# Performance work log

Hardware: AMD Instinct MI355X
Metric: run time of the kernel (lower is better)

## Reference

```python
import jax, jax.numpy as jnp
import numpy as np

B, L, D = 16, 4096, 256
DEP = 50


def setup_inputs() -> dict:
    key = jax.random.key(0)
    ks = jax.random.split(key, 20)
    s = 1.0 / np.sqrt(D)
    inp = {
        "inputs": jax.random.normal(ks[0], (B, L, D), jnp.float32),
        "parent_positions": jax.random.randint(ks[1], (B, L), 0, L, jnp.int32),
        "sentence_deps": jax.random.randint(ks[2], (B, L), 0, DEP, jnp.int32),
        "attention_mask": jax.random.randint(ks[3], (B, L), 0, 2, jnp.int32),
        # linear weights stored [in, out]
        "W_loop": jax.random.uniform(ks[4], (D, D), jnp.float32, -s, s),
        "b_loop": jnp.zeros((D,), jnp.float32),
        "W_child": jax.random.uniform(ks[5], (D, D), jnp.float32, -s, s),
        "b_child": jnp.zeros((D,), jnp.float32),
        "W_parent": jax.random.uniform(ks[6], (D, D), jnp.float32, -s, s),
        "b_parent": jnp.zeros((D,), jnp.float32),
        "w_loop_g": jax.random.uniform(ks[7], (D, 1), jnp.float32, -s, s),
        "b_loop_g": jnp.zeros((1,), jnp.float32),
        "w_child_g": jax.random.uniform(ks[8], (D, 1), jnp.float32, -s, s),
        "b_child_g": jnp.zeros((1,), jnp.float32),
        "w_parent_g": jax.random.uniform(ks[9], (D, 1), jnp.float32, -s, s),
        "b_parent_g": jnp.zeros((1,), jnp.float32),
        "E_pw": jax.random.normal(ks[10], (DEP, D), jnp.float32),
        "E_cw": jax.random.normal(ks[11], (DEP, D), jnp.float32),
        "E_pg": jax.random.normal(ks[12], (DEP, 1), jnp.float32),
        "E_cg": jax.random.normal(ks[13], (DEP, 1), jnp.float32),
    }
    return inp


def _scatter_add_children(idx, vals):
    # idx: [L] parent index per child; vals: [L, D]
    # out[p] = sum_{i: idx[i]==p} vals[i]  (== one_hot(idx).T @ vals)
    return jnp.zeros((L, vals.shape[-1]), vals.dtype).at[idx].add(vals)


def reference(inputs, parent_positions, sentence_deps, attention_mask,
              W_loop, b_loop, W_child, b_child, W_parent, b_parent,
              w_loop_g, b_loop_g, w_child_g, b_child_g, w_parent_g, b_parent_g,
              E_pw, E_cw, E_pg, E_cg):
    x = inputs
    n_iterator = 1
    for _ in range(n_iterator):
        # gather parent node states: [B, L, D]
        par = jnp.take_along_axis(x, parent_positions[:, :, None].astype(jnp.int32), axis=1)
        deps = sentence_deps
        loop_gate = jax.nn.sigmoid(x @ w_loop_g + b_loop_g)                       # [B,L,1]
        par_gate = jax.nn.sigmoid(x @ w_parent_g + b_parent_g + E_pg[deps])       # [B,L,1]
        child_gate = jax.nn.sigmoid(x @ w_child_g + b_child_g + E_cg[deps])       # [B,L,1]
        loop_conv = loop_gate * (x @ W_loop + b_loop)
        parent_conv = par_gate * (par @ W_parent + b_parent + E_pw[deps])
        child_mat = child_gate * (x @ W_child + b_child + E_cw[deps])
        # masked parents (pad positions point to 0), then scatter-add children
        mpp = jnp.where(attention_mask != 0, parent_positions, 0)
        child_conv = jax.vmap(_scatter_add_children)(mpp, child_mat)
        x = loop_conv + parent_conv + child_conv
    return x * attention_mask[:, :, None].astype(x.dtype)
```

## Files before the change

kernel.cpp:

```cpp
#include <hip/hip_runtime.h>
#include <hip/hip_bf16.h>
#include <stdint.h>

#define B_ 16
#define L_ 4096
#define D_ 256
#define M_ (B_*L_)
#define N_ 768

typedef __attribute__((ext_vector_type(8))) short bf16x8;
typedef __attribute__((ext_vector_type(4))) float f32x4;
typedef __attribute__((ext_vector_type(4))) int i32x4;

__device__ __forceinline__ float bf2f(unsigned short u) {
  union { unsigned int i; float f; } v; v.i = ((unsigned int)u) << 16; return v.f;
}
__device__ __forceinline__ unsigned short f2bf(float f) {
  __hip_bfloat16 h = __float2bfloat16(f);
  return *reinterpret_cast<unsigned short*>(&h);
}
__device__ __forceinline__ void async16(const void* g, void* l) {
  __builtin_amdgcn_global_load_lds((const __attribute__((address_space(1))) void*)g,
                                   (__attribute__((address_space(3))) void*)l, 16, 0, 0);
}
__device__ __forceinline__ float sigmoidf_(float z) {
  return 1.f / (1.f + __expf(-z));
}

__global__ __launch_bounds__(256) void k_gates(
    const float* __restrict__ x, const int* __restrict__ deps,
    const int* __restrict__ parent, const int* __restrict__ mask,
    const float* __restrict__ wlg, const float* __restrict__ blg,
    const float* __restrict__ wcg, const float* __restrict__ bcg,
    const float* __restrict__ wpg, const float* __restrict__ bpg,
    const float* __restrict__ Epg, const float* __restrict__ Ecg,
    unsigned short* __restrict__ xb, float4* __restrict__ gates,
    int* __restrict__ cnt)
{
  const int lane = threadIdx.x & 63;
  const int gw = (blockIdx.x * 256 + threadIdx.x) >> 6;
  const float4 wl4 = ((const float4*)wlg)[lane];
  const float4 wc4 = ((const float4*)wcg)[lane];
  const float4 wp4 = ((const float4*)wpg)[lane];
  const float bl0 = blg[0], bc0 = bcg[0], bp0 = bpg[0];
  for (int t = 0; t < 8; ++t) {
    const int i = gw * 8 + t;
    const int b = i >> 12;
    float4 xv = ((const float4*)x)[(size_t)i * 64 + lane];
    float sl = xv.x * wl4.x + xv.y * wl4.y + xv.z * wl4.z + xv.w * wl4.w;
    float sc = xv.x * wc4.x + xv.y * wc4.y + xv.z * wc4.z + xv.w * wc4.w;
    float sp = xv.x * wp4.x + xv.y * wp4.y + xv.z * wp4.z + xv.w * wp4.w;
    #pragma unroll
    for (int o = 32; o; o >>= 1) {
      sl += __shfl_xor(sl, o);
      sc += __shfl_xor(sc, o);
      sp += __shfl_xor(sp, o);
    }
    ushort4 u;
    u.x = f2bf(xv.x); u.y = f2bf(xv.y); u.z = f2bf(xv.z); u.w = f2bf(xv.w);
    ((ushort4*)xb)[(size_t)i * 64 + lane] = u;
    if (lane == 0) {
      int d = deps[i];
      float gl = sigmoidf_(sl + bl0);
      float gp = sigmoidf_(sp + bp0 + Epg[d]);
      float gc = sigmoidf_(sc + bc0 + Ecg[d]);
      gates[i] = make_float4(gl, gp, gc, 0.f);
      int mi = mask[i];
      if (mi) {
        int p = parent[i];
        if (p > 0 && mask[(b << 12) + p]) atomicAdd(&cnt[(b << 12) + p], 1);
      }
    }
  }
}

__global__ __launch_bounds__(256) void k_weights(
    const float* __restrict__ Wl, const float* __restrict__ Wp,
    const float* __restrict__ Wc, unsigned short* __restrict__ WbT)
{
  const int n = blockIdx.x;
  const int k = threadIdx.x;
  const float* W = (n < 256) ? Wl : ((n < 512) ? Wp : Wc);
  const int nn = n & 255;
  WbT[(size_t)n * 256 + k] = f2bf(W[(size_t)k * 256 + nn]);
}

__global__ __launch_bounds__(256) void k_scan(
    const int* __restrict__ cnt, int* __restrict__ off, int* __restrict__ cur)
{
  const int b = blockIdx.x, t = threadIdx.x;
  const int base = (b << 12) + t * 16;
  int v, pre[16], s = 0;
  #pragma unroll
  for (int j = 0; j < 16; ++j) { v = cnt[base + j]; pre[j] = s; s += v; }
  __shared__ int tot[256];
  tot[t] = s;
  __syncthreads();
  for (int o = 1; o < 256; o <<= 1) {
    int x = (t >= o) ? tot[t - o] : 0;
    __syncthreads();
    tot[t] += x;
    __syncthreads();
  }
  const int bexc = tot[t] - s;
  #pragma unroll
  for (int j = 0; j < 16; ++j) {
    off[base + j] = bexc + pre[j];
    cur[base + j] = bexc + pre[j];
  }
}

__global__ __launch_bounds__(256) void k_fill(
    const int* __restrict__ parent, const int* __restrict__ mask,
    int* __restrict__ cur, int* __restrict__ lists)
{
  const int i = blockIdx.x * 256 + threadIdx.x;
  const int b = i >> 12;
  if (!mask[i]) return;
  const int p = parent[i];
  if (p == 0) return;
  if (!mask[(b << 12) + p]) return;
  const int pos = atomicAdd(&cur[(b << 12) + p], 1);
  lists[(b << 12) + pos] = i;
}

__global__ __launch_bounds__(256) void k_gemm(
    const unsigned short* __restrict__ A,
    const unsigned short* __restrict__ Bt,
    unsigned short* __restrict__ Y)
{
  __shared__ unsigned short sh[2 * 128 * 64];
  unsigned short* lA = sh;
  unsigned short* lB = sh + 128 * 64;
  const int tid = threadIdx.x;
  const int wid = tid >> 6, lane = tid & 63;
  const int wm = wid >> 1, wn = wid & 1;
  const int mb = blockIdx.x, nb = blockIdx.y;

  f32x4 acc[4][4] = {};
  const unsigned short* Ag = A + (size_t)mb * 128 * 256;
  const unsigned short* Bg = Bt + (size_t)nb * 128 * 256;
  const int srow = wid * 8 + (lane >> 3);
  const int scol = (lane & 7) * 8;

  for (int kb = 0; kb < 256; kb += 64) {
    #pragma unroll
    for (int s = 0; s < 4; ++s) {
      char* dA = (char*)lA + s * 4096 + wid * 1024 + lane * 16;
      char* dB = (char*)lB + s * 4096 + wid * 1024 + lane * 16;
      async16(Ag + (size_t)(s * 32 + srow) * 256 + kb + scol, dA);
      async16(Bg + (size_t)(s * 32 + srow) * 256 + kb + scol, dB);
    }
    __syncthreads();
    #pragma unroll
    for (int kk = 0; kk < 64; kk += 32) {
      const int ko = kk + (lane >> 4) * 8;
      bf16x8 af[4], bv[4];
      #pragma unroll
      for (int m = 0; m < 4; ++m)
        af[m] = *(const bf16x8*)&lA[(wm * 64 + m * 16 + (lane & 15)) * 64 + ko];
      #pragma unroll
      for (int n = 0; n < 4; ++n)
        bv[n] = *(const bf16x8*)&lB[(wn * 64 + n * 16 + (lane & 15)) * 64 + ko];
      #pragma unroll
      for (int m = 0; m < 4; ++m)
        #pragma unroll
        for (int n = 0; n < 4; ++n)
          acc[m][n] = __builtin_amdgcn_mfma_f32_16x16x32_bf16(af[m], bv[n], acc[m][n], 0, 0, 0);
    }
    __syncthreads();
  }

  #pragma unroll
  for (int m = 0; m < 4; ++m)
    #pragma unroll
    for (int n = 0; n < 4; ++n)
      #pragma unroll
      for (int r = 0; r < 4; ++r)
        sh[(wm * 64 + m * 16 + (lane >> 4) * 4 + r) * 128 + wn * 64 + n * 16 + (lane & 15)]
            = f2bf(acc[m][n][r]);
  __syncthreads();
  #pragma unroll
  for (int s = 0; s < 8; ++s) {
    const int o = s * 4096 + tid * 16;
    const int row = o >> 8;
    const int colu = (o & 255) >> 1;
    *(i32x4*)&Y[(size_t)(mb * 128 + row) * 768 + nb * 128 + colu] =
        *(const i32x4*)((const char*)sh + o);
  }
}

__global__ __launch_bounds__(256) void k_fused(
    const unsigned short* __restrict__ Y, const float4* __restrict__ gates,
    const int* __restrict__ parent, const int* __restrict__ deps,
    const int* __restrict__ mask, const int* __restrict__ cnt,
    const int* __restrict__ off, const int* __restrict__ lists,
    const float* __restrict__ b_loop, const float* __restrict__ b_parent,
    const float* __restrict__ b_child,
    const float* __restrict__ Epw, const float* __restrict__ Ecw,
    float* __restrict__ out)
{
  const int lane = threadIdx.x & 63;
  const int i = blockIdx.x * 4 + (threadIdx.x >> 6);
  const int b = i >> 12;
  float4* orow = (float4*)(out + (size_t)i * 256) + lane;
  if (!mask[i]) { *orow = make_float4(0.f, 0.f, 0.f, 0.f); return; }

  const float4 g = gates[i];
  const int p = parent[i], d = deps[i];
  const float4 bl = ((const float4*)b_loop)[lane];
  const float4 bp = ((const float4*)b_parent)[lane];
  const ushort4 yl = ((const ushort4*)(Y + (size_t)i * 768))[lane];
  const ushort4 z  = ((const ushort4*)(Y + (size_t)((b << 12) + p) * 768 + 256))[lane];
  const float4 e   = ((const float4*)Epw)[d * 64 + lane];
  float4 o;
  o.x = g.x * (bf2f(yl.x) + bl.x) + g.y * (bf2f(z.x) + bp.x + e.x);
  o.y = g.x * (bf2f(yl.y) + bl.y) + g.y * (bf2f(z.y) + bp.y + e.y);
  o.z = g.x * (bf2f(yl.z) + bl.z) + g.y * (bf2f(z.z) + bp.z + e.z);
  o.w = g.x * (bf2f(yl.w) + bl.w) + g.y * (bf2f(z.w) + bp.w + e.w);

  const int n = cnt[i];
  if (n) {
    const int o0 = off[i];
    const float4 bc = ((const float4*)b_child)[lane];
    for (int k = 0; k < n; ++k) {
      const int c = lists[(b << 12) + o0 + k];
      const float gc = ((const float*)gates)[c * 4 + 2];
      const int dc = deps[c];
      const ushort4 yc = ((const ushort4*)(Y + (size_t)c * 768 + 512))[lane];
      const float4 ec = ((const float4*)Ecw)[dc * 64 + lane];
      o.x += gc * (bf2f(yc.x) + bc.x + ec.x);
      o.y += gc * (bf2f(yc.y) + bc.y + ec.y);
      o.z += gc * (bf2f(yc.z) + bc.z + ec.z);
      o.w += gc * (bf2f(yc.w) + bc.w + ec.w);
    }
  }
  *orow = o;
}

__global__ __launch_bounds__(256) void k_row0a(
    const unsigned short* __restrict__ Y, const float4* __restrict__ gates,
    const int* __restrict__ parent, const int* __restrict__ deps,
    const int* __restrict__ mask, const float* __restrict__ b_child,
    const float* __restrict__ Ecw, float4* __restrict__ partial)
{
  const int blk = blockIdx.x;
  const int b = blk >> 6;
  const int lane = threadIdx.x & 63;
  const int wid = threadIdx.x >> 6;
  float4 acc = make_float4(0.f, 0.f, 0.f, 0.f);
  if (mask[b << 12]) {
    const float4 bc = ((const float4*)b_child)[lane];
    const int tbase = (b << 12) + (blk & 63) * 64 + wid * 16;
    for (int t = 0; t < 16; ++t) {
      const int i = tbase + t;
      const int mi = mask[i];
      const int p = parent[i];
      if (mi && p != 0) continue;
      const float gc = ((const float*)gates)[i * 4 + 2];
      const int d = deps[i];
      const ushort4 yc = ((const ushort4*)(Y + (size_t)i * 768 + 512))[lane];
      const float4 ec = ((const float4*)Ecw)[d * 64 + lane];
      acc.x += gc * (bf2f(yc.x) + bc.x + ec.x);
      acc.y += gc * (bf2f(yc.y) + bc.y + ec.y);
      acc.z += gc * (bf2f(yc.z) + bc.z + ec.z);
      acc.w += gc * (bf2f(yc.w) + bc.w + ec.w);
    }
  }
  __shared__ float4 red[4][64];
  red[wid][lane] = acc;
  __syncthreads();
  if (wid == 0) {
    float4 a0 = red[0][lane], a1 = red[1][lane], a2 = red[2][lane], a3 = red[3][lane];
    a0.x += a1.x + a2.x + a3.x;
    a0.y += a1.y + a2.y + a3.y;
    a0.z += a1.z + a2.z + a3.z;
    a0.w += a1.w + a2.w + a3.w;
    partial[blk * 64 + lane] = a0;
  }
}

__global__ __launch_bounds__(64) void k_row0b(
    const int* __restrict__ mask, const float4* __restrict__ partial,
    float* __restrict__ out)
{
  const int b = blockIdx.x;
  if (!mask[b << 12]) return;
  const int t = threadIdx.x;
  float4 acc = make_float4(0.f, 0.f, 0.f, 0.f);
  for (int k = 0; k < 64; ++k) {
    const float4 v = partial[(b * 64 + k) * 64 + t];
    acc.x += v.x; acc.y += v.y; acc.z += v.z; acc.w += v.w;
  }
  float4* orow = (float4*)(out + (size_t)(b << 12) * 256) + t;
  float4 o = *orow;
  o.x += acc.x; o.y += acc.y; o.z += acc.z; o.w += acc.w;
  *orow = o;
}

extern "C" void kernel_launch(void* const* d_in, const int* in_sizes, int n_in,
                              void* d_out, int out_size, void* d_ws, size_t ws_size,
                              hipStream_t stream) {
  const float* x        = (const float*)d_in[0];
  const int*   parent   = (const int*)d_in[1];
  const int*   deps     = (const int*)d_in[2];
  const int*   mask     = (const int*)d_in[3];
  const float* W_loop   = (const float*)d_in[4];
  const float* b_loop   = (const float*)d_in[5];
  const float* W_child  = (const float*)d_in[6];
  const float* b_child  = (const float*)d_in[7];
  const float* W_parent = (const float*)d_in[8];
  const float* b_parent = (const float*)d_in[9];
  const float* wlg      = (const float*)d_in[10];
  const float* blg      = (const float*)d_in[11];
  const float* wcg      = (const float*)d_in[12];
  const float* bcg      = (const float*)d_in[13];
  const float* wpg      = (const float*)d_in[14];
  const float* bpg      = (const float*)d_in[15];
  const float* Epw      = (const float*)d_in[16];
  const float* Ecw      = (const float*)d_in[17];
  const float* Epg      = (const float*)d_in[18];
  const float* Ecg      = (const float*)d_in[19];
  float* out = (float*)d_out;

  char* ws = (char*)d_ws;
  unsigned short* xb  = (unsigned short*)ws;
  float4* partial     = (float4*)ws;
  unsigned short* WbT = (unsigned short*)(ws + 33554432);
  float4* gates       = (float4*)(ws + 33947648);
  unsigned short* Yv  = (unsigned short*)(ws + 34996224);
  int* cnt            = (int*)(ws + 135659520);
  int* off            = (int*)(ws + 135921664);
  int* cur            = (int*)(ws + 136183808);
  int* lists          = (int*)(ws + 136445952);

  hipMemsetAsync(cnt, 0, 262144, stream);
  k_gates<<<2048, 256, 0, stream>>>(x, deps, parent, mask, wlg, blg, wcg, bcg,
                                    wpg, bpg, Epg, Ecg, xb, gates, cnt);
  k_weights<<<768, 256, 0, stream>>>(W_loop, W_parent, W_child, WbT);
  k_scan<<<16, 256, 0, stream>>>(cnt, off, cur);
  k_fill<<<256, 256, 0, stream>>>(parent, mask, cur, lists);
  dim3 gg(512, 6, 1);
  k_gemm<<<gg, 256, 0, stream>>>(xb, WbT, Yv);
  k_row0a<<<1024, 256, 0, stream>>>(Yv, gates, parent, deps, mask, b_child,
                                    Ecw, partial);
  k_fused<<<16384, 256, 0, stream>>>(Yv, gates, parent, deps, mask, cnt, off,
                                     lists, b_loop, b_parent, b_child,
                                     Epw, Ecw, out);
  k_row0b<<<16, 64, 0, stream>>>(mask, partial, out);
}
```

Baseline: 263.8 us.

## Merge preprocessing kernels, build child lists in LDS, reorder GEMM grid

Measured after the change: 343.4 us. +30.1%, slower.

```diff
diff --git a/kernel.cpp b/kernel.cpp
--- a/kernel.cpp
+++ b/kernel.cpp
@@ -27,25 +27,89 @@
   return 1.f / (1.f + __expf(-z));
 }
 
-__global__ __launch_bounds__(256) void k_gates(
+__global__ __launch_bounds__(256) void k_pre(
     const float* __restrict__ x, const int* __restrict__ deps,
     const int* __restrict__ parent, const int* __restrict__ mask,
     const float* __restrict__ wlg, const float* __restrict__ blg,
     const float* __restrict__ wcg, const float* __restrict__ bcg,
     const float* __restrict__ wpg, const float* __restrict__ bpg,
     const float* __restrict__ Epg, const float* __restrict__ Ecg,
+    const float* __restrict__ Wl, const float* __restrict__ Wp,
+    const float* __restrict__ Wc,
     unsigned short* __restrict__ xb, float4* __restrict__ gates,
-    int* __restrict__ cnt)
+    unsigned short* __restrict__ WbT,
+    int* __restrict__ cnt, int* __restrict__ off, int* __restrict__ lists,
+    int* __restrict__ counter)
 {
-  const int lane = threadIdx.x & 63;
-  const int gw = (blockIdx.x * 256 + threadIdx.x) >> 6;
+  __shared__ int hist[4096];
+  __shared__ int tot[256];
+  const int bx = blockIdx.x;
+  const int tid = threadIdx.x;
+
+  if (bx >= 2048) {
+    if (bx < 2816) {
+      const int n = bx - 2048;
+      const float* W = (n < 256) ? Wl : ((n < 512) ? Wp : Wc);
+      WbT[(size_t)n * 256 + tid] = f2bf(W[(size_t)tid * 256 + (n & 255)]);
+    } else if (bx < 2832) {
+      const int b = bx - 2816;
+      const int base = b << 12;
+      #pragma unroll
+      for (int j = 0; j < 16; ++j) hist[tid + j * 256] = 0;
+      __syncthreads();
+      for (int j = 0; j < 16; ++j) {
+        const int i = base + j * 256 + tid;
+        if (mask[i]) {
+          const int p = parent[i];
+          if (p > 0 && mask[base + p]) atomicAdd(&hist[p], 1);
+        }
+      }
+      __syncthreads();
+      int v[16], s = 0;
+      #pragma unroll
+      for (int j = 0; j < 16; ++j) { v[j] = hist[tid * 16 + j]; s += v[j]; }
+      tot[tid] = s;
+      __syncthreads();
+      for (int o = 1; o < 256; o <<= 1) {
+        int xx = (tid >= o) ? tot[tid - o] : 0;
+        __syncthreads();
+        tot[tid] += xx;
+        __syncthreads();
+      }
+      int run = tot[tid] - s;
+      #pragma unroll
+      for (int j = 0; j < 16; ++j) {
+        const int k = tid * 16 + j;
+        cnt[base + k] = v[j];
+        off[base + k] = run;
+        hist[k] = run;
+        run += v[j];
+      }
+      __syncthreads();
+      for (int j = 0; j < 16; ++j) {
+        const int i = base + j * 256 + tid;
+        if (mask[i]) {
+          const int p = parent[i];
+          if (p > 0 && mask[base + p]) {
+            const int pos = atomicAdd(&hist[p], 1);
+            lists[base + pos] = i;
+          }
+        }
+      }
+    } else {
+      if (tid == 0) *counter = 0;
+    }
+    return;
+  }
+
+  const int lane = tid & 63;
+  const int gw = (bx * 256 + tid) >> 6;
   const float4 wl4 = ((const float4*)wlg)[lane];
   const float4 wc4 = ((const float4*)wcg)[lane];
   const float4 wp4 = ((const float4*)wpg)[lane];
   const float bl0 = blg[0], bc0 = bcg[0], bp0 = bpg[0];
   for (int t = 0; t < 8; ++t) {
     const int i = gw * 8 + t;
-    const int b = i >> 12;
     float4 xv = ((const float4*)x)[(size_t)i * 64 + lane];
     float sl = xv.x * wl4.x + xv.y * wl4.y + xv.z * wl4.z + xv.w * wl4.w;
     float sc = xv.x * wc4.x + xv.y * wc4.y + xv.z * wc4.z + xv.w * wc4.w;
@@ -65,63 +129,8 @@
       float gp = sigmoidf_(sp + bp0 + Epg[d]);
       float gc = sigmoidf_(sc + bc0 + Ecg[d]);
       gates[i] = make_float4(gl, gp, gc, 0.f);
-      int mi = mask[i];
-      if (mi) {
-        int p = parent[i];
-        if (p > 0 && mask[(b << 12) + p]) atomicAdd(&cnt[(b << 12) + p], 1);
-      }
-    }
-  }
-}
-
-__global__ __launch_bounds__(256) void k_weights(
-    const float* __restrict__ Wl, const float* __restrict__ Wp,
-    const float* __restrict__ Wc, unsigned short* __restrict__ WbT)
-{
-  const int n = blockIdx.x;
-  const int k = threadIdx.x;
-  const float* W = (n < 256) ? Wl : ((n < 512) ? Wp : Wc);
-  const int nn = n & 255;
-  WbT[(size_t)n * 256 + k] = f2bf(W[(size_t)k * 256 + nn]);
-}
-
-__global__ __launch_bounds__(256) void k_scan(
-    const int* __restrict__ cnt, int* __restrict__ off, int* __restrict__ cur)
-{
-  const int b = blockIdx.x, t = threadIdx.x;
-  const int base = (b << 12) + t * 16;
-  int v, pre[16], s = 0;
-  #pragma unroll
-  for (int j = 0; j < 16; ++j) { v = cnt[base + j]; pre[j] = s; s += v; }
-  __shared__ int tot[256];
-  tot[t] = s;
-  __syncthreads();
-  for (int o = 1; o < 256; o <<= 1) {
-    int x = (t >= o) ? tot[t - o] : 0;
-    __syncthreads();
-    tot[t] += x;
-    __syncthreads();
-  }
-  const int bexc = tot[t] - s;
-  #pragma unroll
-  for (int j = 0; j < 16; ++j) {
-    off[base + j] = bexc + pre[j];
-    cur[base + j] = bexc + pre[j];
-  }
-}
-
-__global__ __launch_bounds__(256) void k_fill(
-    const int* __restrict__ parent, const int* __restrict__ mask,
-    int* __restrict__ cur, int* __restrict__ lists)
-{
-  const int i = blockIdx.x * 256 + threadIdx.x;
-  const int b = i >> 12;
-  if (!mask[i]) return;
-  const int p = parent[i];
-  if (p == 0) return;
-  if (!mask[(b << 12) + p]) return;
-  const int pos = atomicAdd(&cur[(b << 12) + p], 1);
-  lists[(b << 12) + pos] = i;
+    }
+  }
 }
 
 __global__ __launch_bounds__(256) void k_gemm(
@@ -135,7 +144,8 @@
   const int tid = threadIdx.x;
   const int wid = tid >> 6, lane = tid & 63;
   const int wm = wid >> 1, wn = wid & 1;
-  const int mb = blockIdx.x, nb = blockIdx.y;
+  const int bid = blockIdx.x;
+  const int mb = bid / 6, nb = bid % 6;
 
   f32x4 acc[4][4] = {};
   const unsigned short* Ag = A + (size_t)mb * 128 * 256;
@@ -238,11 +248,12 @@
   *orow = o;
 }
 
-__global__ __launch_bounds__(256) void k_row0a(
+__global__ __launch_bounds__(256) void k_row0(
     const unsigned short* __restrict__ Y, const float4* __restrict__ gates,
     const int* __restrict__ parent, const int* __restrict__ deps,
     const int* __restrict__ mask, const float* __restrict__ b_child,
-    const float* __restrict__ Ecw, float4* __restrict__ partial)
+    const float* __restrict__ Ecw, float4* __restrict__ partial,
+    int* __restrict__ counter, float* __restrict__ out)
 {
   const int blk = blockIdx.x;
   const int b = blk >> 6;
@@ -268,6 +279,7 @@
     }
   }
   __shared__ float4 red[4][64];
+  __shared__ int lastflag;
   red[wid][lane] = acc;
   __syncthreads();
   if (wid == 0) {
@@ -278,24 +290,26 @@
     a0.w += a1.w + a2.w + a3.w;
     partial[blk * 64 + lane] = a0;
   }
-}
-
-__global__ __launch_bounds__(64) void k_row0b(
-    const int* __restrict__ mask, const float4* __restrict__ partial,
-    float* __restrict__ out)
-{
-  const int b = blockIdx.x;
-  if (!mask[b << 12]) return;
-  const int t = threadIdx.x;
-  float4 acc = make_float4(0.f, 0.f, 0.f, 0.f);
-  for (int k = 0; k < 64; ++k) {
-    const float4 v = partial[(b * 64 + k) * 64 + t];
-    acc.x += v.x; acc.y += v.y; acc.z += v.z; acc.w += v.w;
-  }
-  float4* orow = (float4*)(out + (size_t)(b << 12) * 256) + t;
-  float4 o = *orow;
-  o.x += acc.x; o.y += acc.y; o.z += acc.z; o.w += acc.w;
-  *orow = o;
+  __threadfence();
+  __syncthreads();
+  if (threadIdx.x == 0)
+    lastflag = (atomicAdd(counter, 1) == 1023);
+  __syncthreads();
+  if (!lastflag) return;
+  __threadfence();
+  for (int w = threadIdx.x; w < 1024; w += 256) {
+    const int bb = w >> 6, c = w & 63;
+    if (!mask[bb << 12]) continue;
+    float4 s = make_float4(0.f, 0.f, 0.f, 0.f);
+    for (int k = 0; k < 64; ++k) {
+      const float4 v = partial[(bb * 64 + k) * 64 + c];
+      s.x += v.x; s.y += v.y; s.z += v.z; s.w += v.w;
+    }
+    float4* orow = (float4*)(out + (size_t)(bb << 12) * 256) + c;
+    float4 o = *orow;
+    o.x += s.x; o.y += s.y; o.z += s.z; o.w += s.w;
+    *orow = o;
+  }
 }
 
 extern "C" void kernel_launch(void* const* d_in, const int* in_sizes, int n_in,
@@ -331,21 +345,16 @@
   unsigned short* Yv  = (unsigned short*)(ws + 34996224);
   int* cnt            = (int*)(ws + 135659520);
   int* off            = (int*)(ws + 135921664);
-  int* cur            = (int*)(ws + 136183808);
-  int* lists          = (int*)(ws + 136445952);
-
-  hipMemsetAsync(cnt, 0, 262144, stream);
-  k_gates<<<2048, 256, 0, stream>>>(x, deps, parent, mask, wlg, blg, wcg, bcg,
-                                    wpg, bpg, Epg, Ecg, xb, gates, cnt);
-  k_weights<<<768, 256, 0, stream>>>(W_loop, W_parent, W_child, WbT);
-  k_scan<<<16, 256, 0, stream>>>(cnt, off, cur);
-  k_fill<<<256, 256, 0, stream>>>(parent, mask, cur, lists);
-  dim3 gg(512, 6, 1);
-  k_gemm<<<gg, 256, 0, stream>>>(xb, WbT, Yv);
-  k_row0a<<<1024, 256, 0, stream>>>(Yv, gates, parent, deps, mask, b_child,
-                                    Ecw, partial);
+  int* lists          = (int*)(ws + 136183808);
+  int* counter        = (int*)(ws + 136445952);
+
+  k_pre<<<2833, 256, 0, stream>>>(x, deps, parent, mask, wlg, blg, wcg, bcg,
+                                  wpg, bpg, Epg, Ecg, W_loop, W_parent, W_child,
+                                  xb, gates, WbT, cnt, off, lists, counter);
+  k_gemm<<<3072, 256, 0, stream>>>(xb, WbT, Yv);
   k_fused<<<16384, 256, 0, stream>>>(Yv, gates, parent, deps, mask, cnt, off,
                                      lists, b_loop, b_parent, b_child,
                                      Epw, Ecw, out);
-  k_row0b<<<16, 64, 0, stream>>>(mask, partial, out);
-}
+  k_row0<<<1024, 256, 0, stream>>>(Yv, gates, parent, deps, mask, b_child,
+                                   Ecw, partial, counter, out);
+}
```
